# Optimization experiments

Measured on AMD Instinct MI355X. Metric: run time of the kernel, lower is better.

Reference implementation:

```python
import jax, jax.numpy as jnp
import numpy as np

# Semantic hierarchy configuration (stand-in for semantic_softmax_processor)
GROUP_SIZES = [8192, 4096, 2048, 1024, 512, 256, 128, 64, 32, 16]
NORM_FACTORS = [0.1] * len(GROUP_SIZES)
TOPK_CAP = 500
TEMPERATURE = 1.0
TOTAL_CLASSES = sum(GROUP_SIZES)  # 16368
BATCH = 1024


def setup_inputs() -> dict:
    key = jax.random.key(0)
    k1, k2, k3 = jax.random.split(key, 3)
    logits = jax.random.normal(k1, (BATCH, TOTAL_CLASSES), dtype=jnp.float32)
    logits_teacher = jax.random.normal(k2, (BATCH, TOTAL_CLASSES), dtype=jnp.float32)
    targets = jax.random.randint(k3, (BATCH,), 0, TOTAL_CLASSES, dtype=jnp.int64)
    return {"logits": logits, "logits_teacher": logits_teacher, "targets": targets}


def _group_kd_loss(s_logits, t_logits, temperature):
    # s_logits, t_logits: [B, C_i] for one semantic group
    B, C = t_logits.shape
    k = min(C, TOPK_CAP)
    # teacher top-k classes (sorted, largest)
    t_top, t_idx = jax.lax.top_k(t_logits, k)                 # [B, k]
    s_top = jnp.take_along_axis(s_logits, t_idx, axis=1)      # [B, k]
    log_p = jax.nn.log_softmax(s_top / temperature, axis=1)   # student log-probs
    log_q = jax.nn.log_softmax(t_top / temperature, axis=1)   # teacher log-probs
    q = jnp.exp(log_q)
    # KL(q || p), reduction='batchmean'
    kl = jnp.sum(q * (log_q - log_p)) / B
    return kl * temperature * temperature


def reference(logits, logits_teacher, targets):
    # targets are converted to semantic targets in the original module but are
    # never used in the loss computation (dead code) -> no effect on output.
    del targets
    total = jnp.float32(0.0)
    offset = 0
    for gsize, norm in zip(GROUP_SIZES, NORM_FACTORS):
        s_i = jax.lax.slice_in_dim(logits, offset, offset + gsize, axis=1)
        t_i = jax.lax.slice_in_dim(logits_teacher, offset, offset + gsize, axis=1)
        total = total + _group_kd_loss(s_i, t_i, TEMPERATURE) * norm
        offset += gsize
    return total
```

## Files before the change

kernel.cpp:

```cpp
#include <hip/hip_runtime.h>
#include <stdint.h>
#include <float.h>

#define TOTAL 16368
#define KSEL 500
#define CAP 1280
#define NSLOT 20
#define NBUCKET 64

__device__ __forceinline__ uint32_t fkey(float f) {
    uint32_t u = __float_as_uint(f);
    return (u & 0x80000000u) ? ~u : (u | 0x80000000u);
}
__device__ __forceinline__ float keyf(uint32_t k) {
    uint32_t u = (k & 0x80000000u) ? (k & 0x7FFFFFFFu) : ~k;
    return __uint_as_float(u);
}
__device__ __forceinline__ int lanerank(uint64_t m) {
    return __builtin_amdgcn_mbcnt_hi((uint32_t)(m >> 32),
           __builtin_amdgcn_mbcnt_lo((uint32_t)m, 0));
}
__device__ __forceinline__ int wave_sumi(int v) {
    #pragma unroll
    for (int o = 32; o > 0; o >>= 1) v += __shfl_xor(v, o, 64);
    return v;
}
__device__ __forceinline__ float wave_sumf(float v) {
    #pragma unroll
    for (int o = 32; o > 0; o >>= 1) v += __shfl_xor(v, o, 64);
    return v;
}
__device__ __forceinline__ float wave_maxf(float v) {
    #pragma unroll
    for (int o = 32; o > 0; o >>= 1) v = fmaxf(v, __shfl_xor(v, o, 64));
    return v;
}
__device__ __forceinline__ void lse_merge(float& m, float& l, float m2, float l2) {
    float M = fmaxf(m, m2);
    l = l * __expf(m - M) + l2 * __expf(m2 - M);
    m = M;
}

__device__ __noinline__ float wave_slow_kl(const float* __restrict__ t,
                                           const float* __restrict__ s, int C) {
    const int lane = threadIdx.x & 63;
    uint64_t lo = 0ull, hi = (1ull << 45), tau = 0ull;
    int cl = C, ch = 0;
    #pragma unroll 1
    for (int it = 0; it < 100; ++it) {
        uint64_t span = hi - lo;
        if (span <= 1ull) { tau = lo; break; }
        uint64_t mid;
        if (it & 1) mid = lo + (span >> 1);
        else {
            uint64_t st = span * (uint64_t)(cl - KSEL) / (uint64_t)(cl - ch);
            if (st < 1) st = 1;
            if (st > span - 1) st = span - 1;
            mid = lo + st;
        }
        int c = 0;
        #pragma unroll 1
        for (int i = lane; i < C; i += 64) {
            uint64_t ck = ((uint64_t)fkey(t[i]) << 13) | (uint64_t)(8191 - i);
            c += (ck > mid);
        }
        c = wave_sumi(c);
        if (c == KSEL) { tau = mid; break; }
        if (c > KSEL) { lo = mid; cl = c; } else { hi = mid; ch = c; }
    }
    float tmx = -FLT_MAX;
    for (int i = lane; i < C; i += 64) tmx = fmaxf(tmx, t[i]);
    tmx = wave_maxf(tmx);
    float St = 0.f, Stt = 0.f, Sts = 0.f, sm = -FLT_MAX;
    #pragma unroll 1
    for (int i = lane; i < C; i += 64) {
        float x = t[i];
        uint64_t ck = ((uint64_t)fkey(x) << 13) | (uint64_t)(8191 - i);
        if (ck > tau) {
            float e = __expf(x - tmx), v = s[i];
            St += e; Stt += e * x; Sts += e * v;
            sm = fmaxf(sm, v);
        }
    }
    St = wave_sumf(St); Stt = wave_sumf(Stt); Sts = wave_sumf(Sts); sm = wave_maxf(sm);
    float Ss = 0.f;
    #pragma unroll 1
    for (int i = lane; i < C; i += 64) {
        uint64_t ck = ((uint64_t)fkey(t[i]) << 13) | (uint64_t)(8191 - i);
        if (ck > tau) Ss += __expf(s[i] - sm);
    }
    Ss = wave_sumf(Ss);
    if (lane == 0)
        return (Stt - Sts) / St - tmx - __logf(St) + sm + __logf(Ss);
    return 0.f;
}

template <int NF4>
__device__ float big_wave(const float* __restrict__ tg, const float* __restrict__ s,
                          float thr, float* vals, uint16_t* idxs) {
    const int lane = threadIdx.x & 63;
    const float4* t4 = (const float4*)tg;
    constexpr int NB = NF4 / 8;
    int cnt = 0;
    float4 buf[8], nxt[8];
    #pragma unroll
    for (int u = 0; u < 8; ++u) buf[u] = t4[u * 64 + lane];
    #pragma unroll 1
    for (int b = 0; b < NB; ++b) {
        if (b + 1 < NB) {
            #pragma unroll
            for (int u = 0; u < 8; ++u)
                nxt[u] = t4[((b + 1) * 8 + u) * 64 + lane];
        }
        #pragma unroll
        for (int u = 0; u < 8; ++u) {
            float xs[4] = {buf[u].x, buf[u].y, buf[u].z, buf[u].w};
            #pragma unroll
            for (int q = 0; q < 4; ++q) {
                bool p = xs[q] > thr;
                uint64_t m = __ballot(p);
                if (p) {
                    int ofs = cnt + lanerank(m);
                    if (ofs < CAP) {
                        vals[ofs] = xs[q];
                        idxs[ofs] = (uint16_t)((((b * 8 + u) * 64 + lane) << 2) + q);
                    }
                }
                cnt += (int)__popcll(m);
            }
        }
        if (b + 1 < NB) {
            #pragma unroll
            for (int u = 0; u < 8; ++u) buf[u] = nxt[u];
        }
    }
    if (cnt < KSEL || cnt > CAP) return wave_slow_kl(tg, s, NF4 * 256);

    uint32_t key[NSLOT];
    float svc[NSLOT];
    #pragma unroll
    for (int j = 0; j < NSLOT; ++j) {
        int p = lane + j * 64;
        bool v = p < cnt;
        key[j] = v ? fkey(vals[p]) : 0u;
        svc[j] = v ? s[(int)idxs[p]] : 0.f;
    }
    uint32_t kmx = 0u, kmn = 0xFFFFFFFFu;
    #pragma unroll
    for (int j = 0; j < NSLOT; ++j) {
        uint32_t k = key[j];
        kmx = k > kmx ? k : kmx;
        if (k) kmn = k < kmn ? k : kmn;
    }
    #pragma unroll
    for (int o = 32; o > 0; o >>= 1) {
        uint32_t a = __shfl_xor(kmx, o, 64); kmx = a > kmx ? a : kmx;
        uint32_t b2 = __shfl_xor(kmn, o, 64); kmn = b2 < kmn ? b2 : kmn;
    }
    const float tmax = keyf(kmx);

    uint32_t lo = kmn - 1u, hi = kmx, tauhi = kmx;
    int cl = cnt, ch = 0, cut = -1;
    bool exact = false;
    #pragma unroll 1
    for (int it = 0; it < 80; ++it) {
        uint32_t span = hi - lo;
        if (span <= 1u) break;
        uint32_t mid;
        if (!(it & 1)) {
            uint64_t st = (uint64_t)span * (uint32_t)(cl - KSEL) / (uint32_t)(cl - ch);
            if (st < 1) st = 1;
            if (st > span - 1) st = span - 1;
            mid = lo + (uint32_t)st;
        } else mid = lo + (span >> 1);
        int c = 0;
        #pragma unroll
        for (int j = 0; j < NSLOT; ++j)
            c += (int)__popcll(__ballot(key[j] > mid));
        if (c == KSEL) { tauhi = mid; exact = true; break; }
        if (c > KSEL) { lo = mid; cl = c; } else { hi = mid; ch = c; }
    }
    if (!exact) {
        tauhi = hi;
        const int nT = KSEL - ch, nTie = cl - ch;
        if (nT >= nTie) cut = 0x7FFFFFFF;
        else {
            int idxr[NSLOT];
            #pragma unroll
            for (int j = 0; j < NSLOT; ++j) {
                int p = lane + j * 64;
                idxr[j] = (p < cnt) ? (int)idxs[p] : 0x7FFF;
            }
            int l = -1, h = 8191;
            #pragma unroll 1
            while (h - l > 1) {
                int m = (l + h) >> 1;
                int c = 0;
                #pragma unroll
                for (int j = 0; j < NSLOT; ++j)
                    c += (int)__popcll(__ballot(key[j] == tauhi && idxr[j] <= m));
                if (c >= nT) h = m; else l = m;
            }
            cut = h;
        }
    }

    uint32_t selm = 0u;
    if (cut == -1) {
        #pragma unroll
        for (int j = 0; j < NSLOT; ++j) selm |= (key[j] > tauhi ? 1u : 0u) << j;
    } else if (cut == 0x7FFFFFFF) {
        #pragma unroll
        for (int j = 0; j < NSLOT; ++j) selm |= (key[j] >= tauhi ? 1u : 0u) << j;
    } else {
        #pragma unroll
        for (int j = 0; j < NSLOT; ++j) {
            int p = lane + j * 64;
            bool sj = (key[j] > tauhi) ||
                      (key[j] == tauhi && p < cnt && (int)idxs[p] <= cut);
            selm |= (sj ? 1u : 0u) << j;
        }
    }

    float St = 0.f, Stt = 0.f, Sts = 0.f, sm = -FLT_MAX;
    #pragma unroll
    for (int j = 0; j < NSLOT; ++j) {
        if (selm & (1u << j)) {
            float tv = keyf(key[j]);
            float e = __expf(tv - tmax);
            St += e; Stt += e * tv; Sts += e * svc[j];
            sm = fmaxf(sm, svc[j]);
        }
    }
    #pragma unroll
    for (int o = 32; o > 0; o >>= 1) {
        St  += __shfl_xor(St,  o, 64);
        Stt += __shfl_xor(Stt, o, 64);
        Sts += __shfl_xor(Sts, o, 64);
        sm = fmaxf(sm, __shfl_xor(sm, o, 64));
    }
    float Ss = 0.f;
    #pragma unroll
    for (int j = 0; j < NSLOT; ++j)
        if (selm & (1u << j)) Ss += __expf(svc[j] - sm);
    Ss = wave_sumf(Ss);
    if (lane == 0)
        return (Stt - Sts) / St - tmax - __logf(St) + sm + __logf(Ss);
    return 0.f;
}

template <int NS, class IdxF>
__device__ float select_accum(uint32_t (&key)[NS], IdxF idxOf, const float* svp) {
    const int lane = threadIdx.x & 63;
    uint32_t kmx = 0u, kmn = 0xFFFFFFFFu;
    #pragma unroll
    for (int j = 0; j < NS; ++j) {
        uint32_t k = key[j];
        kmx = k > kmx ? k : kmx;
        kmn = k < kmn ? k : kmn;
    }
    #pragma unroll
    for (int o = 32; o > 0; o >>= 1) {
        uint32_t a = __shfl_xor(kmx, o, 64); kmx = a > kmx ? a : kmx;
        uint32_t b = __shfl_xor(kmn, o, 64); kmn = b < kmn ? b : kmn;
    }
    const float tmax = keyf(kmx);

    uint32_t lo = kmn - 1u, hi = kmx, tauhi = kmx;
    int cl = NS * 64, ch = 0, cut = -1;
    bool exact = false;
    #pragma unroll 1
    for (int it = 0; it < 80; ++it) {
        uint32_t span = hi - lo;
        if (span <= 1u) break;
        uint32_t mid;
        if (!(it & 1)) {
            uint64_t st = (uint64_t)span * (uint32_t)(cl - KSEL) / (uint32_t)(cl - ch);
            if (st < 1) st = 1;
            if (st > span - 1) st = span - 1;
            mid = lo + (uint32_t)st;
        } else mid = lo + (span >> 1);
        int c = 0;
        #pragma unroll
        for (int j = 0; j < NS; ++j)
            c += (int)__popcll(__ballot(key[j] > mid));
        if (c == KSEL) { tauhi = mid; exact = true; break; }
        if (c > KSEL) { lo = mid; cl = c; } else { hi = mid; ch = c; }
    }
    if (!exact) {
        tauhi = hi;
        const int nT = KSEL - ch, nTie = cl - ch;
        if (nT >= nTie) cut = 0x7FFFFFFF;
        else {
            int l = -1, h = NS * 64 - 1;
            #pragma unroll 1
            while (h - l > 1) {
                int m = (l + h) >> 1;
                int c = 0;
                #pragma unroll
                for (int j = 0; j < NS; ++j)
                    c += (int)__popcll(__ballot(key[j] == tauhi && idxOf(j) <= m));
                if (c >= nT) h = m; else l = m;
            }
            cut = h;
        }
    }

    float St = 0.f, Stt = 0.f, Sts = 0.f, sm = -FLT_MAX;
    #pragma unroll
    for (int j = 0; j < NS; ++j) {
        uint32_t kj = key[j];
        bool sj = (kj > tauhi) || (kj == tauhi && idxOf(j) <= cut);
        if (sj) {
            float tv = keyf(kj);
            float e = __expf(tv - tmax);
            St += e; Stt += e * tv; Sts += e * svp[j];
            sm = fmaxf(sm, svp[j]);
        }
    }
    #pragma unroll
    for (int o = 32; o > 0; o >>= 1) {
        St  += __shfl_xor(St,  o, 64);
        Stt += __shfl_xor(Stt, o, 64);
        Sts += __shfl_xor(Sts, o, 64);
        sm = fmaxf(sm, __shfl_xor(sm, o, 64));
    }
    float Ss = 0.f;
    #pragma unroll
    for (int j = 0; j < NS; ++j) {
        uint32_t kj = key[j];
        bool sj = (kj > tauhi) || (kj == tauhi && idxOf(j) <= cut);
        if (sj) Ss += __expf(svp[j] - sm);
    }
    Ss = wave_sumf(Ss);
    if (lane == 0)
        return (Stt - Sts) / St - tmax - __logf(St) + sm + __logf(Ss);
    return 0.f;
}

template <int NJ>
__device__ float mid_wave(const float* __restrict__ t, const float* __restrict__ s) {
    const int lane = threadIdx.x & 63;
    const float4* t4 = (const float4*)t;
    const float4* s4 = (const float4*)s;
    uint32_t key[NJ];
    float svp[NJ];
    #pragma unroll
    for (int c = 0; c < NJ / 4; ++c) {
        float4 x = t4[lane + c * 64];
        float4 y = s4[lane + c * 64];
        key[4 * c + 0] = fkey(x.x); key[4 * c + 1] = fkey(x.y);
        key[4 * c + 2] = fkey(x.z); key[4 * c + 3] = fkey(x.w);
        svp[4 * c + 0] = y.x; svp[4 * c + 1] = y.y;
        svp[4 * c + 2] = y.z; svp[4 * c + 3] = y.w;
    }
    auto idxOf = [&](int j) { return ((lane + (j >> 2) * 64) << 2) + (j & 3); };
    return select_accum<NJ>(key, idxOf, svp);
}

__device__ float tiny_group(const float* __restrict__ t, const float* __restrict__ s,
                            int Cg) {
    const int lane = threadIdx.x & 63;
    float St = 0.f, Stt = 0.f, Sts = 0.f, m = -FLT_MAX, l = 0.f;
    float tv[4], svv[4];
    #pragma unroll
    for (int q = 0; q < 4; ++q) {
        int i = lane + q * 64;
        bool va = i < Cg;
        tv[q] = va ? t[i] : -FLT_MAX;
        svv[q] = va ? s[i] : 0.f;
    }
    float mx = -FLT_MAX;
    #pragma unroll
    for (int q = 0; q < 4; ++q) mx = fmaxf(mx, tv[q]);
    mx = wave_maxf(mx);
    #pragma unroll
    for (int q = 0; q < 4; ++q) {
        if (lane + q * 64 < Cg) {
            float e = __expf(tv[q] - mx);
            St += e; Stt += e * tv[q]; Sts += e * svv[q];
            float x = svv[q];
            if (x > m) { l = l * __expf(m - x) + 1.f; m = x; }
            else       { l += __expf(x - m); }
        }
    }
    #pragma unroll
    for (int o = 32; o > 0; o >>= 1) {
        St  += __shfl_xor(St,  o, 64);
        Stt += __shfl_xor(Stt, o, 64);
        Sts += __shfl_xor(Sts, o, 64);
        float m2 = __shfl_xor(m, o, 64);
        float l2 = __shfl_xor(l, o, 64);
        lse_merge(m, l, m2, l2);
    }
    if (lane == 0)
        return (Stt - Sts) / St - mx - __logf(St) + m + __logf(l);
    return 0.f;
}

__global__ __launch_bounds__(64, 4) void kd_jobs(const float* __restrict__ sL,
                                                 const float* __restrict__ tL,
                                                 float* __restrict__ partial) {
    __shared__ float    vals[CAP];
    __shared__ uint16_t idxs[CAP];
    const int bid = blockIdx.x;
    const int job = bid >> 10;
    const int row = bid & 1023;
    const float* tr = tL + (size_t)row * TOTAL;
    const float* sr = sL + (size_t)row * TOTAL;

    float kl = 0.f;
    switch (job) {
    case 0:
        kl = big_wave<32>(tr, sr, 1.10f, vals, idxs);
        break;
    case 1:
        kl = big_wave<16>(tr + 8192, sr + 8192, 0.60f, vals, idxs);
        break;
    case 2:
        kl  = big_wave<8>(tr + 12288, sr + 12288, 0.50f, vals, idxs);
        kl += mid_wave<16>(tr + 14336, sr + 14336);
        break;
    default:
        kl  = mid_wave<8>(tr + 15360, sr + 15360);
        kl += tiny_group(tr + 15872, sr + 15872, 256);
        kl += tiny_group(tr + 16128, sr + 16128, 128);
        kl += tiny_group(tr + 16256, sr + 16256, 64);
        kl += tiny_group(tr + 16320, sr + 16320, 32);
        kl += tiny_group(tr + 16352, sr + 16352, 16);
        break;
    }

    if ((threadIdx.x & 63) == 0)
        atomicAdd(&partial[(row + job * 37) & (NBUCKET - 1)], kl * (0.1f / 1024.f));
}

__global__ void zero_ws(float* partial) {
    if (threadIdx.x < NBUCKET) partial[threadIdx.x] = 0.f;
}

__global__ void final_sum(const float* __restrict__ partial, float* __restrict__ out) {
    float v = (threadIdx.x < NBUCKET) ? partial[threadIdx.x] : 0.f;
    #pragma unroll
    for (int o = 32; o > 0; o >>= 1) v += __shfl_down(v, o, 64);
    if (threadIdx.x == 0) out[0] = v;
}

extern "C" void kernel_launch(void* const* d_in, const int* in_sizes, int n_in,
                              void* d_out, int out_size, void* d_ws, size_t ws_size,
                              hipStream_t stream) {
    (void)in_sizes; (void)n_in; (void)ws_size; (void)out_size;
    const float* s = (const float*)d_in[0];
    const float* t = (const float*)d_in[1];
    float* out = (float*)d_out;
    float* ws = (float*)d_ws;

    hipLaunchKernelGGL(zero_ws, dim3(1), dim3(64), 0, stream, ws);
    hipLaunchKernelGGL(kd_jobs, dim3(4096), dim3(64), 0, stream, s, t, ws);
    hipLaunchKernelGGL(final_sum, dim3(1), dim3(64), 0, stream, ws, out);
}
```

Measured before the change: 167.4 us.

## Stream student logits with teacher, drop index gather, split job 2 into two

```diff
diff --git a/kernel.cpp b/kernel.cpp
--- a/kernel.cpp
+++ b/kernel.cpp
@@ -4,7 +4,7 @@
 
 #define TOTAL 16368
 #define KSEL 500
-#define CAP 1280
+#define CAPV 1280
 #define NSLOT 20
 #define NBUCKET 64
 
@@ -96,54 +96,56 @@
 }
 
 template <int NF4>
-__device__ float big_wave(const float* __restrict__ tg, const float* __restrict__ s,
-                          float thr, float* vals, uint16_t* idxs) {
+__device__ float big_wave(const float* __restrict__ tg, const float* __restrict__ sg,
+                          float thr, uint32_t* kv, float* sv) {
     const int lane = threadIdx.x & 63;
     const float4* t4 = (const float4*)tg;
-    constexpr int NB = NF4 / 8;
+    const float4* s4 = (const float4*)sg;
+    constexpr int NB = NF4 / 4;
+    constexpr int C = NF4 * 256;
     int cnt = 0;
-    float4 buf[8], nxt[8];
-    #pragma unroll
-    for (int u = 0; u < 8; ++u) buf[u] = t4[u * 64 + lane];
+    float4 tb[4], sb[4], tn[4], sn[4];
+    #pragma unroll
+    for (int u = 0; u < 4; ++u) { tb[u] = t4[u * 64 + lane]; sb[u] = s4[u * 64 + lane]; }
     #pragma unroll 1
     for (int b = 0; b < NB; ++b) {
         if (b + 1 < NB) {
             #pragma unroll
-            for (int u = 0; u < 8; ++u)
-                nxt[u] = t4[((b + 1) * 8 + u) * 64 + lane];
+            for (int u = 0; u < 4; ++u) {
+                tn[u] = t4[((b + 1) * 4 + u) * 64 + lane];
+                sn[u] = s4[((b + 1) * 4 + u) * 64 + lane];
+            }
         }
         #pragma unroll
-        for (int u = 0; u < 8; ++u) {
-            float xs[4] = {buf[u].x, buf[u].y, buf[u].z, buf[u].w};
+        for (int u = 0; u < 4; ++u) {
+            float tx[4] = {tb[u].x, tb[u].y, tb[u].z, tb[u].w};
+            float sx[4] = {sb[u].x, sb[u].y, sb[u].z, sb[u].w};
             #pragma unroll
             for (int q = 0; q < 4; ++q) {
-                bool p = xs[q] > thr;
+                bool p = tx[q] > thr;
                 uint64_t m = __ballot(p);
                 if (p) {
                     int ofs = cnt + lanerank(m);
-                    if (ofs < CAP) {
-                        vals[ofs] = xs[q];
-                        idxs[ofs] = (uint16_t)((((b * 8 + u) * 64 + lane) << 2) + q);
-                    }
+                    if (ofs < CAPV) { kv[ofs] = fkey(tx[q]); sv[ofs] = sx[q]; }
                 }
                 cnt += (int)__popcll(m);
             }
         }
         if (b + 1 < NB) {
             #pragma unroll
-            for (int u = 0; u < 8; ++u) buf[u] = nxt[u];
-        }
-    }
-    if (cnt < KSEL || cnt > CAP) return wave_slow_kl(tg, s, NF4 * 256);
-
+            for (int u = 0; u < 4; ++u) { tb[u] = tn[u]; sb[u] = sn[u]; }
+        }
+    }
+    if (cnt < KSEL || cnt > CAPV) return wave_slow_kl(tg, sg, C);
+
+    for (int p = cnt + lane; p < CAPV; p += 64) kv[p] = 0u;
     uint32_t key[NSLOT];
     float svc[NSLOT];
     #pragma unroll
     for (int j = 0; j < NSLOT; ++j) {
         int p = lane + j * 64;
-        bool v = p < cnt;
-        key[j] = v ? fkey(vals[p]) : 0u;
-        svc[j] = v ? s[(int)idxs[p]] : 0.f;
+        key[j] = kv[p];
+        svc[j] = (p < cnt) ? sv[p] : 0.f;
     }
     uint32_t kmx = 0u, kmn = 0xFFFFFFFFu;
     #pragma unroll
@@ -160,8 +162,9 @@
     const float tmax = keyf(kmx);
 
     uint32_t lo = kmn - 1u, hi = kmx, tauhi = kmx;
-    int cl = cnt, ch = 0, cut = -1;
-    bool exact = false;
+    int cl = cnt, ch = 0;
+    bool exact = false, tiesAll = false;
+    int tieN = 0;
     #pragma unroll 1
     for (int it = 0; it < 80; ++it) {
         uint32_t span = hi - lo;
@@ -183,53 +186,36 @@
     if (!exact) {
         tauhi = hi;
         const int nT = KSEL - ch, nTie = cl - ch;
-        if (nT >= nTie) cut = 0x7FFFFFFF;
-        else {
-            int idxr[NSLOT];
-            #pragma unroll
-            for (int j = 0; j < NSLOT; ++j) {
-                int p = lane + j * 64;
-                idxr[j] = (p < cnt) ? (int)idxs[p] : 0x7FFF;
-            }
-            int l = -1, h = 8191;
-            #pragma unroll 1
-            while (h - l > 1) {
-                int m = (l + h) >> 1;
-                int c = 0;
-                #pragma unroll
-                for (int j = 0; j < NSLOT; ++j)
-                    c += (int)__popcll(__ballot(key[j] == tauhi && idxr[j] <= m));
-                if (c >= nT) h = m; else l = m;
-            }
-            cut = h;
-        }
-    }
-
-    uint32_t selm = 0u;
-    if (cut == -1) {
-        #pragma unroll
-        for (int j = 0; j < NSLOT; ++j) selm |= (key[j] > tauhi ? 1u : 0u) << j;
-    } else if (cut == 0x7FFFFFFF) {
-        #pragma unroll
-        for (int j = 0; j < NSLOT; ++j) selm |= (key[j] >= tauhi ? 1u : 0u) << j;
-    } else {
-        #pragma unroll
-        for (int j = 0; j < NSLOT; ++j) {
-            int p = lane + j * 64;
-            bool sj = (key[j] > tauhi) ||
-                      (key[j] == tauhi && p < cnt && (int)idxs[p] <= cut);
-            selm |= (sj ? 1u : 0u) << j;
-        }
+        if (nT >= nTie) tiesAll = true;
+        else tieN = nT;
     }
 
     float St = 0.f, Stt = 0.f, Sts = 0.f, sm = -FLT_MAX;
     #pragma unroll
     for (int j = 0; j < NSLOT; ++j) {
-        if (selm & (1u << j)) {
+        bool sj = tiesAll ? (key[j] >= tauhi) : (key[j] > tauhi);
+        if (sj) {
             float tv = keyf(key[j]);
             float e = __expf(tv - tmax);
             St += e; Stt += e * tv; Sts += e * svc[j];
             sm = fmaxf(sm, svc[j]);
+        }
+    }
+    if (tieN > 0) {
+        int rem = tieN;
+        #pragma unroll 1
+        for (int base = 0; base < C && rem > 0; base += 64) {
+            float tvv = tg[base + lane];
+            bool tie = (fkey(tvv) == tauhi);
+            uint64_t m = __ballot(tie);
+            if (tie && lanerank(m) < rem) {
+                float e = __expf(tvv - tmax);
+                float svv = sg[base + lane];
+                St += e; Stt += e * tvv; Sts += e * svv;
+                sm = fmaxf(sm, svv);
+            }
+            int pc = (int)__popcll(m);
+            rem = (pc >= rem) ? 0 : (rem - pc);
         }
     }
     #pragma unroll
@@ -241,8 +227,23 @@
     }
     float Ss = 0.f;
     #pragma unroll
-    for (int j = 0; j < NSLOT; ++j)
-        if (selm & (1u << j)) Ss += __expf(svc[j] - sm);
+    for (int j = 0; j < NSLOT; ++j) {
+        bool sj = tiesAll ? (key[j] >= tauhi) : (key[j] > tauhi);
+        if (sj) Ss += __expf(svc[j] - sm);
+    }
+    if (tieN > 0) {
+        int rem = tieN;
+        #pragma unroll 1
+        for (int base = 0; base < C && rem > 0; base += 64) {
+            float tvv = tg[base + lane];
+            bool tie = (fkey(tvv) == tauhi);
+            uint64_t m = __ballot(tie);
+            if (tie && lanerank(m) < rem)
+                Ss += __expf(sg[base + lane] - sm);
+            int pc = (int)__popcll(m);
+            rem = (pc >= rem) ? 0 : (rem - pc);
+        }
+    }
     Ss = wave_sumf(Ss);
     if (lane == 0)
         return (Stt - Sts) / St - tmax - __logf(St) + sm + __logf(Ss);
@@ -401,8 +402,8 @@
 __global__ __launch_bounds__(64, 4) void kd_jobs(const float* __restrict__ sL,
                                                  const float* __restrict__ tL,
                                                  float* __restrict__ partial) {
-    __shared__ float    vals[CAP];
-    __shared__ uint16_t idxs[CAP];
+    __shared__ uint32_t kv[CAPV];
+    __shared__ float    sv[CAPV];
     const int bid = blockIdx.x;
     const int job = bid >> 10;
     const int row = bid & 1023;
@@ -412,14 +413,16 @@
     float kl = 0.f;
     switch (job) {
     case 0:
-        kl = big_wave<32>(tr, sr, 1.10f, vals, idxs);
+        kl = big_wave<32>(tr, sr, 1.10f, kv, sv);
         break;
     case 1:
-        kl = big_wave<16>(tr + 8192, sr + 8192, 0.60f, vals, idxs);
+        kl = big_wave<16>(tr + 8192, sr + 8192, 0.60f, kv, sv);
         break;
     case 2:
-        kl  = big_wave<8>(tr + 12288, sr + 12288, 0.50f, vals, idxs);
-        kl += mid_wave<16>(tr + 14336, sr + 14336);
+        kl = big_wave<8>(tr + 12288, sr + 12288, 0.50f, kv, sv);
+        break;
+    case 3:
+        kl = mid_wave<16>(tr + 14336, sr + 14336);
         break;
     default:
         kl  = mid_wave<8>(tr + 15360, sr + 15360);
@@ -456,6 +459,6 @@
     float* ws = (float*)d_ws;
 
     hipLaunchKernelGGL(zero_ws, dim3(1), dim3(64), 0, stream, ws);
-    hipLaunchKernelGGL(kd_jobs, dim3(4096), dim3(64), 0, stream, s, t, ws);
+    hipLaunchKernelGGL(kd_jobs, dim3(5120), dim3(64), 0, stream, s, t, ws);
     hipLaunchKernelGGL(final_sum, dim3(1), dim3(64), 0, stream, ws, out);
 }
```

Result: slower. 171.8 us (+2.6%).
